# Kernel tuning notes

Hardware: AMD Instinct MI355X
Metric: run time of the kernel (lower is better)

## Reference

```python
import jax, jax.numpy as jnp
import numpy as np

H, C = 8, 8  # num_heads, c_hidden; c_m = H*C = 64
LN_EPS = 1e-5


def setup_inputs() -> dict:
    key = jax.random.key(0)
    ks = jax.random.split(key, 8)
    B, S, L, CM = 2, 512, 384, H * C
    m = jax.random.normal(ks[0], (B, S, L, CM), dtype=jnp.float32)
    msa_mask = jax.random.randint(ks[1], (B, S, L), 0, 2).astype(jnp.float32)
    sc = 1.0 / np.sqrt(CM)
    return {
        "m": m,
        "msa_mask": msa_mask,
        "ln_w": jnp.ones((CM,), jnp.float32),
        "ln_b": jnp.zeros((CM,), jnp.float32),
        "wq": jax.random.normal(ks[2], (CM, H * C), jnp.float32) * sc,
        "wk": jax.random.normal(ks[3], (CM, H * C), jnp.float32) * sc,
        "wv": jax.random.normal(ks[4], (CM, H * C), jnp.float32) * sc,
        "wg": jax.random.normal(ks[5], (CM, H * C), jnp.float32) * sc,
        "bg": jnp.ones((H * C,), jnp.float32),
        "wo": jax.random.normal(ks[6], (H * C, CM), jnp.float32) * sc,
        "bo": jnp.zeros((CM,), jnp.float32),
    }


def reference(m, msa_mask, ln_w, ln_b, wq, wk, wv, wg, bg, wo, bo):
    B, S, L, CM = m.shape
    # LayerNorm over c_m
    mu = jnp.mean(m, axis=-1, keepdims=True)
    var = jnp.mean(jnp.square(m - mu), axis=-1, keepdims=True)
    x = (m - mu) * jax.lax.rsqrt(var + LN_EPS) * ln_w + ln_b

    k = (x @ wk).reshape(B, S, L, H, C)
    v = (x @ wv).reshape(B, S, L, H, C)
    g = jax.nn.sigmoid(x @ wg + bg).reshape(B, S, L, H, C)

    # masked mean over the sequence axis S -> global query per residue
    denom = jnp.maximum(jnp.sum(msa_mask, axis=1), 1.0)  # [B, L]
    q_input = jnp.sum(x * msa_mask[..., None], axis=1) / denom[..., None]  # [B, L, CM]
    q = (q_input @ wq).reshape(B, L, H, C)

    logits = jnp.einsum("blhc,bslhc->blhs", q, k) / np.sqrt(C).astype(np.float32)
    mask_bls = jnp.transpose(msa_mask, (0, 2, 1))[:, :, None, :]  # [B, L, 1, S]
    logits = jnp.where(mask_bls == 0, -1e9, logits)
    attn = jax.nn.softmax(logits, axis=-1)  # [B, L, H, S]

    out_global = jnp.einsum("blhs,bslhc->blhc", attn, v)  # [B, L, H, C]
    out = g * out_global[:, None]  # broadcast over S -> [B, S, L, H, C]
    out = out.reshape(B, S, L, H * C) @ wo + bo
    out = out * msa_mask[..., None]
    return out
```

## Files before the change

### kernel.cpp

```cpp
#include <hip/hip_runtime.h>

#define NH 8
#define DCM 64
#define NB 2
#define NS 512
#define NL 384
#define LN_EPS 1e-5f
#define INV_SQRT_C 0.35355339059327379f

typedef __attribute__((ext_vector_type(8))) short short8v;
typedef __attribute__((ext_vector_type(4))) float f32x4;

__device__ __forceinline__ float4 ld4(const float* p) {
  return *reinterpret_cast<const float4*>(p);
}
__device__ __forceinline__ unsigned short f2bf(float f) {
  unsigned int b = __float_as_uint(f);
  b += 0x7FFFu + ((b >> 16) & 1u);
  return (unsigned short)(b >> 16);
}
__device__ __forceinline__ float bf2f(unsigned short u) {
  return __uint_as_float(((unsigned int)u) << 16);
}

__global__ void prep_weights(const float* __restrict__ wg,
                             const float* __restrict__ wo,
                             const float* __restrict__ wv,
                             unsigned short* __restrict__ wt) {
  int i = blockIdx.x * 256 + threadIdx.x;
  if (i < 4096) {
    int n = i >> 6, k = i & 63;
    wt[i]        = f2bf(wg[k * DCM + n]);
    wt[4096 + i] = f2bf(wo[k * DCM + n]);
    wt[8192 + i] = f2bf(wv[k * DCM + n]);
  }
}

__global__ __launch_bounds__(512, 2) void fused(
    const float* __restrict__ m, const float* __restrict__ msk,
    const float* __restrict__ lnw, const float* __restrict__ lnb,
    const float* __restrict__ wq, const float* __restrict__ wk,
    const unsigned short* __restrict__ wt,
    const float* __restrict__ bg, const float* __restrict__ bo,
    float* __restrict__ out)
{
  const int col = blockIdx.x;
  const int b = col / NL, l = col % NL;
  const int tid = threadIdx.x;
  const int wave = tid >> 6, lane = tid & 63;

  __shared__ __align__(16) unsigned short x_lds[NS * DCM];
  __shared__ __align__(16) unsigned short mask_s[NS];
  __shared__ __align__(16) unsigned char scratch[10752];
  __shared__ __align__(16) unsigned short qk_bf[16 * DCM];

  float* redf  = (float*)scratch;
  float* dredf = redf + 512;
  float* qinf  = redf + 528;
  float* qsf   = redf + 592;
  unsigned short* P_T = (unsigned short*)scratch;
  float* ogredf = (float*)(scratch + 8192);
  float* smredf = (float*)(scratch + 10240);
  float* ogsf   = (float*)(scratch + 10496);

  for (int i = tid; i < NS; i += 512)
    mask_s[i] = f2bf(msk[(b * NS + i) * NL + l]);

  const int c8 = lane & 7;
  const int r8 = lane >> 3;
  float lw8[8], lb8[8];
#pragma unroll
  for (int k = 0; k < 8; ++k) { lw8[k] = lnw[c8 * 8 + k]; lb8[k] = lnb[c8 * 8 + k]; }
  __syncthreads();

  float qacc[8] = {0.f,0.f,0.f,0.f,0.f,0.f,0.f,0.f};
  float dacc = 0.f;
  const int rowbase = wave * 64;
  {
    const size_t rstep = (size_t)8 * NL * DCM;
    const float* mb = m + ((size_t)b * NS * NL + l) * DCM + c8 * 8
                    + (size_t)(rowbase + r8) * NL * DCM;
    auto process = [&](const float4& A, const float4& Bv, int s) {
      float xv[8] = {A.x, A.y, A.z, A.w, Bv.x, Bv.y, Bv.z, Bv.w};
      float s1 = 0.f, s2 = 0.f;
#pragma unroll
      for (int k = 0; k < 8; ++k) { s1 += xv[k]; s2 += xv[k] * xv[k]; }
#pragma unroll
      for (int o = 1; o <= 4; o <<= 1) { s1 += __shfl_xor(s1, o); s2 += __shfl_xor(s2, o); }
      const float mu = s1 * 0.015625f;
      const float rs = rsqrtf(s2 * 0.015625f - mu * mu + LN_EPS);
      const float mk = bf2f(mask_s[s]);
      short8v xp;
#pragma unroll
      for (int k = 0; k < 8; ++k) {
        float xn = (xv[k] - mu) * rs * lw8[k] + lb8[k];
        xp[k] = (short)f2bf(xn);
        qacc[k] += xn * mk;
      }
      dacc += mk;
      *reinterpret_cast<short8v*>(&x_lds[s * DCM + ((c8 * 8) ^ ((s & 7) << 3))]) = xp;
    };
    float4 f0a = ld4(mb),             f0b = ld4(mb + 4);
    float4 f1a = ld4(mb + rstep),     f1b = ld4(mb + rstep + 4);
    float4 f2a = ld4(mb + 2 * rstep), f2b = ld4(mb + 2 * rstep + 4);
    float4 f3a = ld4(mb + 3 * rstep), f3b = ld4(mb + 3 * rstep + 4);
#pragma unroll
    for (int blk = 0; blk < 2; ++blk) {
      const int it0 = blk * 4;
      process(f0a, f0b, rowbase + (it0 + 0) * 8 + r8);
      if (blk < 1) { f0a = ld4(mb + (size_t)(it0 + 4) * rstep);
                     f0b = ld4(mb + (size_t)(it0 + 4) * rstep + 4); }
      process(f1a, f1b, rowbase + (it0 + 1) * 8 + r8);
      if (blk < 1) { f1a = ld4(mb + (size_t)(it0 + 5) * rstep);
                     f1b = ld4(mb + (size_t)(it0 + 5) * rstep + 4); }
      process(f2a, f2b, rowbase + (it0 + 2) * 8 + r8);
      if (blk < 1) { f2a = ld4(mb + (size_t)(it0 + 6) * rstep);
                     f2b = ld4(mb + (size_t)(it0 + 6) * rstep + 4); }
      process(f3a, f3b, rowbase + (it0 + 3) * 8 + r8);
      if (blk < 1) { f3a = ld4(mb + (size_t)(it0 + 7) * rstep);
                     f3b = ld4(mb + (size_t)(it0 + 7) * rstep + 4); }
    }
  }
#pragma unroll
  for (int o = 8; o <= 32; o <<= 1) {
#pragma unroll
    for (int k = 0; k < 8; ++k) qacc[k] += __shfl_xor(qacc[k], o);
    dacc += __shfl_xor(dacc, o);
  }
  if (lane < 8) {
    float4 t0; t0.x = qacc[0]; t0.y = qacc[1]; t0.z = qacc[2]; t0.w = qacc[3];
    float4 t1; t1.x = qacc[4]; t1.y = qacc[5]; t1.z = qacc[6]; t1.w = qacc[7];
    *reinterpret_cast<float4*>(&redf[wave * DCM + lane * 8])     = t0;
    *reinterpret_cast<float4*>(&redf[wave * DCM + lane * 8 + 4]) = t1;
  }
  if (lane == 0) dredf[wave] = dacc;
  __syncthreads();

  if (tid < DCM) {
    float dn = 0.f, a = 0.f;
#pragma unroll
    for (int w = 0; w < 8; ++w) { dn += dredf[w]; a += redf[w * DCM + tid]; }
    qinf[tid] = a / fmaxf(dn, 1.0f);
  }
  __syncthreads();
  if (tid < DCM) {
    float a = 0.f;
    for (int j = 0; j < DCM; ++j) a += qinf[j] * wq[j * DCM + tid];
    qsf[tid] = a;
  }
  __syncthreads();
  for (int idx = tid; idx < 16 * DCM; idx += 512) {
    int h = idx >> 6, cm = idx & 63;
    float a = 0.f;
    if (h < NH) {
#pragma unroll
      for (int c = 0; c < 8; ++c) a += qsf[h * 8 + c] * wk[cm * DCM + h * 8 + c];
      a *= INV_SQRT_C;
    }
    qk_bf[idx] = f2bf(a);
  }
  __syncthreads();

  const int bcol = lane & 15;
  const int kg = lane >> 4;
  short8v qkB0 = *reinterpret_cast<const short8v*>(&qk_bf[bcol * DCM + kg * 8]);
  short8v qkB1 = *reinterpret_cast<const short8v*>(&qk_bf[bcol * DCM + 32 + kg * 8]);
  short8v wvB[4][2];
#pragma unroll
  for (int nt = 0; nt < 4; ++nt)
#pragma unroll
    for (int kw = 0; kw < 2; ++kw)
      wvB[nt][kw] = *reinterpret_cast<const short8v*>(
          &wt[8192 + (nt * 16 + bcol) * DCM + kw * 32 + kg * 8]);
  float smacc = 0.f;
  float ogacc[4] = {0.f, 0.f, 0.f, 0.f};
  for (int t = 0; t < 4; ++t) {
    const int tilebase = rowbase + t * 16;
    const int arow = tilebase + bcol;
    const int swz = (arow & 7) << 3;
    short8v a0 = *reinterpret_cast<const short8v*>(&x_lds[arow * DCM + ((kg * 8) ^ swz)]);
    short8v a1 = *reinterpret_cast<const short8v*>(&x_lds[arow * DCM + ((32 + kg * 8) ^ swz)]);
    f32x4 L = (f32x4){0.f, 0.f, 0.f, 0.f};
    L = __builtin_amdgcn_mfma_f32_16x16x32_bf16(a0, qkB0, L, 0, 0, 0);
    L = __builtin_amdgcn_mfma_f32_16x16x32_bf16(a1, qkB1, L, 0, 0, 0);
    const int s0 = tilebase + kg * 4;
    short4 mk4 = *reinterpret_cast<const short4*>(&mask_s[s0]);
    float p0 = bf2f((unsigned short)mk4.x) * __expf(L[0]);
    float p1 = bf2f((unsigned short)mk4.y) * __expf(L[1]);
    float p2 = bf2f((unsigned short)mk4.z) * __expf(L[2]);
    float p3 = bf2f((unsigned short)mk4.w) * __expf(L[3]);
    smacc += (p0 + p1) + (p2 + p3);
    if (bcol < NH) {
      short4 pw;
      pw.x = (short)f2bf(p0); pw.y = (short)f2bf(p1);
      pw.z = (short)f2bf(p2); pw.w = (short)f2bf(p3);
      *reinterpret_cast<short4*>(&P_T[bcol * NS + (s0 ^ (bcol << 3))]) = pw;
    }
    f32x4 V[4];
#pragma unroll
    for (int nt = 0; nt < 4; ++nt) {
      V[nt] = (f32x4){0.f, 0.f, 0.f, 0.f};
      V[nt] = __builtin_amdgcn_mfma_f32_16x16x32_bf16(a0, wvB[nt][0], V[nt], 0, 0, 0);
      V[nt] = __builtin_amdgcn_mfma_f32_16x16x32_bf16(a1, wvB[nt][1], V[nt], 0, 0, 0);
    }
#pragma unroll
    for (int nt = 0; nt < 4; ++nt) {
      const int h2 = 2 * nt + (bcol >> 3);
      short4 p4 = *reinterpret_cast<const short4*>(&P_T[h2 * NS + (s0 ^ (h2 << 3))]);
      ogacc[nt] += bf2f((unsigned short)p4.x) * V[nt][0]
                 + bf2f((unsigned short)p4.y) * V[nt][1]
                 + bf2f((unsigned short)p4.z) * V[nt][2]
                 + bf2f((unsigned short)p4.w) * V[nt][3];
    }
  }
  smacc += __shfl_xor(smacc, 16); smacc += __shfl_xor(smacc, 32);
  if (lane < NH) smredf[wave * NH + lane] = smacc;
#pragma unroll
  for (int nt = 0; nt < 4; ++nt) {
    ogacc[nt] += __shfl_xor(ogacc[nt], 16);
    ogacc[nt] += __shfl_xor(ogacc[nt], 32);
  }
  if (lane < 16) {
#pragma unroll
    for (int nt = 0; nt < 4; ++nt) ogredf[wave * DCM + nt * 16 + lane] = ogacc[nt];
  }
  __syncthreads();
  if (tid < DCM) {
    float smT = 0.f, a = 0.f;
#pragma unroll
    for (int w = 0; w < 8; ++w) {
      smT += smredf[w * NH + (tid >> 3)];
      a += ogredf[w * DCM + tid];
    }
    ogsf[tid] = a / fmaxf(smT, 1e-30f);
  }
  __syncthreads();

  short8v wgB[4][2], woB[4][2];
  float bgv[4], bov[4], ogv[4];
#pragma unroll
  for (int nt = 0; nt < 4; ++nt) {
    const int ncol = nt * 16 + bcol;
#pragma unroll
    for (int kw = 0; kw < 2; ++kw) {
      wgB[nt][kw] = *reinterpret_cast<const short8v*>(&wt[ncol * DCM + kw * 32 + kg * 8]);
      woB[nt][kw] = *reinterpret_cast<const short8v*>(&wt[4096 + ncol * DCM + kw * 32 + kg * 8]);
    }
    bgv[nt] = bg[ncol]; bov[nt] = bo[ncol]; ogv[nt] = ogsf[ncol];
  }
  const size_t outbase = ((size_t)b * NS * NL + l) * DCM;

  for (int t = 0; t < 4; ++t) {
    const int tilebase = rowbase + t * 16;
    const int arow = tilebase + bcol;
    const int swz = (arow & 7) << 3;
    short8v a0 = *reinterpret_cast<const short8v*>(&x_lds[arow * DCM + ((kg * 8) ^ swz)]);
    short8v a1 = *reinterpret_cast<const short8v*>(&x_lds[arow * DCM + ((32 + kg * 8) ^ swz)]);
    f32x4 accG[4];
#pragma unroll
    for (int nt = 0; nt < 4; ++nt) {
      accG[nt] = (f32x4){0.f, 0.f, 0.f, 0.f};
      accG[nt] = __builtin_amdgcn_mfma_f32_16x16x32_bf16(a0, wgB[nt][0], accG[nt], 0, 0, 0);
      accG[nt] = __builtin_amdgcn_mfma_f32_16x16x32_bf16(a1, wgB[nt][1], accG[nt], 0, 0, 0);
    }
#pragma unroll
    for (int nt = 0; nt < 4; ++nt) {
      const int cc = nt * 16 + bcol;
#pragma unroll
      for (int r = 0; r < 4; ++r) {
        const int r2 = kg * 4 + r;
        float gx = accG[nt][r] + bgv[nt];
        float g = 1.0f / (1.0f + __expf(-gx));
        x_lds[(tilebase + r2) * DCM + (cc ^ ((r2 & 7) << 3))] = f2bf(g * ogv[nt]);
      }
    }
    short8v b0 = *reinterpret_cast<const short8v*>(
        &x_lds[(tilebase + bcol) * DCM + ((kg * 8) ^ ((bcol & 7) << 3))]);
    short8v b1 = *reinterpret_cast<const short8v*>(
        &x_lds[(tilebase + bcol) * DCM + ((32 + kg * 8) ^ ((bcol & 7) << 3))]);
    f32x4 accO[4];
#pragma unroll
    for (int nt = 0; nt < 4; ++nt) {
      accO[nt] = (f32x4){0.f, 0.f, 0.f, 0.f};
      accO[nt] = __builtin_amdgcn_mfma_f32_16x16x32_bf16(b0, woB[nt][0], accO[nt], 0, 0, 0);
      accO[nt] = __builtin_amdgcn_mfma_f32_16x16x32_bf16(b1, woB[nt][1], accO[nt], 0, 0, 0);
    }
#pragma unroll
    for (int nt = 0; nt < 4; ++nt) {
#pragma unroll
      for (int r = 0; r < 4; ++r) {
        const int orow = tilebase + kg * 4 + r;
        const float mk = bf2f(mask_s[orow]);
        out[outbase + (size_t)orow * NL * DCM + nt * 16 + bcol] = (accO[nt][r] + bov[nt]) * mk;
      }
    }
  }
}

extern "C" void kernel_launch(void* const* d_in, const int* in_sizes, int n_in,
                              void* d_out, int out_size, void* d_ws, size_t ws_size,
                              hipStream_t stream) {
  (void)in_sizes; (void)n_in; (void)out_size; (void)ws_size;
  const float* m   = (const float*)d_in[0];
  const float* msk = (const float*)d_in[1];
  const float* lnw = (const float*)d_in[2];
  const float* lnb = (const float*)d_in[3];
  const float* wq  = (const float*)d_in[4];
  const float* wk  = (const float*)d_in[5];
  const float* wv  = (const float*)d_in[6];
  const float* wg  = (const float*)d_in[7];
  const float* bg  = (const float*)d_in[8];
  const float* wo  = (const float*)d_in[9];
  const float* bo  = (const float*)d_in[10];
  unsigned short* wt = (unsigned short*)d_ws;
  float* out = (float*)d_out;

  prep_weights<<<dim3(16), dim3(256), 0, stream>>>(wg, wo, wv, wt);
  fused<<<dim3(NB * NL), dim3(512), 0, stream>>>(
      m, msk, lnw, lnb, wq, wk, wt, bg, bo, out);
}
```

Baseline: 79.77 us.

## Precompute fused Wq·Wk product, row-per-thread LayerNorm, halve block size

Precomputes the combined query-key projection matrix (wq times per-head wk, scaled) in the prep kernel, so the fused kernel turns the masked-mean input into qk logit weights with one 64x512 matvec and no serial wq/wk passes. LayerNorm is rewritten so each thread owns one full row (16 float4 loads) with no shuffle reductions. The masked query sum is recomputed from the bf16 x_lds. Blocks shrink from 512 to 256 threads with each wave covering 128 rows. This trades per-row shuffle work and extra syncs for more register pressure and lower bf16 precision in q_input.

```diff
diff --git a/kernel.cpp b/kernel.cpp
--- a/kernel.cpp
+++ b/kernel.cpp
@@ -23,10 +23,10 @@
   return __uint_as_float(((unsigned int)u) << 16);
 }
 
-__global__ void prep_weights(const float* __restrict__ wg,
-                             const float* __restrict__ wo,
-                             const float* __restrict__ wv,
-                             unsigned short* __restrict__ wt) {
+__global__ void prep(const float* __restrict__ wg, const float* __restrict__ wo,
+                     const float* __restrict__ wv, const float* __restrict__ wq,
+                     const float* __restrict__ wk,
+                     unsigned short* __restrict__ wt, float* __restrict__ Mg) {
   int i = blockIdx.x * 256 + threadIdx.x;
   if (i < 4096) {
     int n = i >> 6, k = i & 63;
@@ -34,13 +34,19 @@
     wt[4096 + i] = f2bf(wo[k * DCM + n]);
     wt[8192 + i] = f2bf(wv[k * DCM + n]);
   }
-}
-
-__global__ __launch_bounds__(512, 2) void fused(
+  if (i < 32768) {
+    int j = i >> 9, idx = i & 511, h = idx >> 6, cm = idx & 63;
+    float a = 0.f;
+#pragma unroll
+    for (int c = 0; c < 8; ++c) a += wq[j * DCM + h * 8 + c] * wk[cm * DCM + h * 8 + c];
+    Mg[i] = a * INV_SQRT_C;
+  }
+}
+
+__global__ __launch_bounds__(256, 4) void fused(
     const float* __restrict__ m, const float* __restrict__ msk,
     const float* __restrict__ lnw, const float* __restrict__ lnb,
-    const float* __restrict__ wq, const float* __restrict__ wk,
-    const unsigned short* __restrict__ wt,
+    const unsigned short* __restrict__ wt, const float* __restrict__ Mg,
     const float* __restrict__ bg, const float* __restrict__ bo,
     float* __restrict__ out)
 {
@@ -51,118 +57,94 @@
 
   __shared__ __align__(16) unsigned short x_lds[NS * DCM];
   __shared__ __align__(16) unsigned short mask_s[NS];
-  __shared__ __align__(16) unsigned char scratch[10752];
+  __shared__ __align__(16) unsigned char scratch[9728];
   __shared__ __align__(16) unsigned short qk_bf[16 * DCM];
 
   float* redf  = (float*)scratch;
-  float* dredf = redf + 512;
-  float* qinf  = redf + 528;
-  float* qsf   = redf + 592;
+  float* dredf = (float*)(scratch + 1024);
   unsigned short* P_T = (unsigned short*)scratch;
   float* ogredf = (float*)(scratch + 8192);
-  float* smredf = (float*)(scratch + 10240);
-  float* ogsf   = (float*)(scratch + 10496);
-
-  for (int i = tid; i < NS; i += 512)
+  float* smredf = (float*)(scratch + 9216);
+  float* ogsf   = (float*)(scratch + 9344);
+
+  for (int i = tid; i < NS; i += 256)
     mask_s[i] = f2bf(msk[(b * NS + i) * NL + l]);
 
-  const int c8 = lane & 7;
-  const int r8 = lane >> 3;
-  float lw8[8], lb8[8];
-#pragma unroll
-  for (int k = 0; k < 8; ++k) { lw8[k] = lnw[c8 * 8 + k]; lb8[k] = lnb[c8 * 8 + k]; }
-  __syncthreads();
-
-  float qacc[8] = {0.f,0.f,0.f,0.f,0.f,0.f,0.f,0.f};
-  float dacc = 0.f;
-  const int rowbase = wave * 64;
+#pragma unroll 1
+  for (int rr = 0; rr < 2; ++rr) {
+    const int r = tid + rr * 256;
+    const float* rp = m + ((size_t)(b * NS + r) * NL + l) * DCM;
+    float4 f[16];
+#pragma unroll
+    for (int j = 0; j < 16; ++j) f[j] = ld4(rp + j * 4);
+    float s1 = 0.f, s2 = 0.f;
+#pragma unroll
+    for (int j = 0; j < 16; ++j) {
+      s1 += (f[j].x + f[j].y) + (f[j].z + f[j].w);
+      s2 = fmaf(f[j].x, f[j].x, s2); s2 = fmaf(f[j].y, f[j].y, s2);
+      s2 = fmaf(f[j].z, f[j].z, s2); s2 = fmaf(f[j].w, f[j].w, s2);
+    }
+    const float mu = s1 * 0.015625f;
+    const float rs = rsqrtf(s2 * 0.015625f - mu * mu + LN_EPS);
+    const int swz = (r & 7) << 3;
+#pragma unroll
+    for (int j = 0; j < 8; ++j) {
+      const float v[8] = {f[2*j].x, f[2*j].y, f[2*j].z, f[2*j].w,
+                          f[2*j+1].x, f[2*j+1].y, f[2*j+1].z, f[2*j+1].w};
+      short8v xp;
+#pragma unroll
+      for (int k = 0; k < 8; ++k)
+        xp[k] = (short)f2bf((v[k] - mu) * rs * lnw[8*j+k] + lnb[8*j+k]);
+      *reinterpret_cast<short8v*>(&x_lds[r * DCM + ((j * 8) ^ swz)]) = xp;
+    }
+  }
+  __syncthreads();
+
+  const int qd = lane & 15, rsub = lane >> 4;
   {
-    const size_t rstep = (size_t)8 * NL * DCM;
-    const float* mb = m + ((size_t)b * NS * NL + l) * DCM + c8 * 8
-                    + (size_t)(rowbase + r8) * NL * DCM;
-    auto process = [&](const float4& A, const float4& Bv, int s) {
-      float xv[8] = {A.x, A.y, A.z, A.w, Bv.x, Bv.y, Bv.z, Bv.w};
-      float s1 = 0.f, s2 = 0.f;
-#pragma unroll
-      for (int k = 0; k < 8; ++k) { s1 += xv[k]; s2 += xv[k] * xv[k]; }
-#pragma unroll
-      for (int o = 1; o <= 4; o <<= 1) { s1 += __shfl_xor(s1, o); s2 += __shfl_xor(s2, o); }
-      const float mu = s1 * 0.015625f;
-      const float rs = rsqrtf(s2 * 0.015625f - mu * mu + LN_EPS);
+    float q0 = 0.f, q1 = 0.f, q2 = 0.f, q3 = 0.f, da = 0.f;
+    for (int it = 0; it < 32; ++it) {
+      const int s = wave * 4 + rsub + it * 16;
+      short4 xv4 = *reinterpret_cast<const short4*>(
+          &x_lds[s * DCM + ((qd * 4) ^ ((s & 7) << 3))]);
       const float mk = bf2f(mask_s[s]);
-      short8v xp;
-#pragma unroll
-      for (int k = 0; k < 8; ++k) {
-        float xn = (xv[k] - mu) * rs * lw8[k] + lb8[k];
-        xp[k] = (short)f2bf(xn);
-        qacc[k] += xn * mk;
-      }
-      dacc += mk;
-      *reinterpret_cast<short8v*>(&x_lds[s * DCM + ((c8 * 8) ^ ((s & 7) << 3))]) = xp;
-    };
-    float4 f0a = ld4(mb),             f0b = ld4(mb + 4);
-    float4 f1a = ld4(mb + rstep),     f1b = ld4(mb + rstep + 4);
-    float4 f2a = ld4(mb + 2 * rstep), f2b = ld4(mb + 2 * rstep + 4);
-    float4 f3a = ld4(mb + 3 * rstep), f3b = ld4(mb + 3 * rstep + 4);
-#pragma unroll
-    for (int blk = 0; blk < 2; ++blk) {
-      const int it0 = blk * 4;
-      process(f0a, f0b, rowbase + (it0 + 0) * 8 + r8);
-      if (blk < 1) { f0a = ld4(mb + (size_t)(it0 + 4) * rstep);
-                     f0b = ld4(mb + (size_t)(it0 + 4) * rstep + 4); }
-      process(f1a, f1b, rowbase + (it0 + 1) * 8 + r8);
-      if (blk < 1) { f1a = ld4(mb + (size_t)(it0 + 5) * rstep);
-                     f1b = ld4(mb + (size_t)(it0 + 5) * rstep + 4); }
-      process(f2a, f2b, rowbase + (it0 + 2) * 8 + r8);
-      if (blk < 1) { f2a = ld4(mb + (size_t)(it0 + 6) * rstep);
-                     f2b = ld4(mb + (size_t)(it0 + 6) * rstep + 4); }
-      process(f3a, f3b, rowbase + (it0 + 3) * 8 + r8);
-      if (blk < 1) { f3a = ld4(mb + (size_t)(it0 + 7) * rstep);
-                     f3b = ld4(mb + (size_t)(it0 + 7) * rstep + 4); }
-    }
-  }
-#pragma unroll
-  for (int o = 8; o <= 32; o <<= 1) {
-#pragma unroll
-    for (int k = 0; k < 8; ++k) qacc[k] += __shfl_xor(qacc[k], o);
-    dacc += __shfl_xor(dacc, o);
-  }
-  if (lane < 8) {
-    float4 t0; t0.x = qacc[0]; t0.y = qacc[1]; t0.z = qacc[2]; t0.w = qacc[3];
-    float4 t1; t1.x = qacc[4]; t1.y = qacc[5]; t1.z = qacc[6]; t1.w = qacc[7];
-    *reinterpret_cast<float4*>(&redf[wave * DCM + lane * 8])     = t0;
-    *reinterpret_cast<float4*>(&redf[wave * DCM + lane * 8 + 4]) = t1;
-  }
-  if (lane == 0) dredf[wave] = dacc;
-  __syncthreads();
-
-  if (tid < DCM) {
-    float dn = 0.f, a = 0.f;
-#pragma unroll
-    for (int w = 0; w < 8; ++w) { dn += dredf[w]; a += redf[w * DCM + tid]; }
-    qinf[tid] = a / fmaxf(dn, 1.0f);
-  }
-  __syncthreads();
-  if (tid < DCM) {
-    float a = 0.f;
-    for (int j = 0; j < DCM; ++j) a += qinf[j] * wq[j * DCM + tid];
-    qsf[tid] = a;
-  }
-  __syncthreads();
-  for (int idx = tid; idx < 16 * DCM; idx += 512) {
-    int h = idx >> 6, cm = idx & 63;
-    float a = 0.f;
-    if (h < NH) {
-#pragma unroll
-      for (int c = 0; c < 8; ++c) a += qsf[h * 8 + c] * wk[cm * DCM + h * 8 + c];
-      a *= INV_SQRT_C;
-    }
-    qk_bf[idx] = f2bf(a);
+      q0 = fmaf(mk, bf2f((unsigned short)xv4.x), q0);
+      q1 = fmaf(mk, bf2f((unsigned short)xv4.y), q1);
+      q2 = fmaf(mk, bf2f((unsigned short)xv4.z), q2);
+      q3 = fmaf(mk, bf2f((unsigned short)xv4.w), q3);
+      da += mk;
+    }
+    q0 += __shfl_xor(q0, 16); q0 += __shfl_xor(q0, 32);
+    q1 += __shfl_xor(q1, 16); q1 += __shfl_xor(q1, 32);
+    q2 += __shfl_xor(q2, 16); q2 += __shfl_xor(q2, 32);
+    q3 += __shfl_xor(q3, 16); q3 += __shfl_xor(q3, 32);
+    da += __shfl_xor(da, 16); da += __shfl_xor(da, 32);
+    if (lane < 16) {
+      float4 t; t.x = q0; t.y = q1; t.z = q2; t.w = q3;
+      *reinterpret_cast<float4*>(&redf[wave * DCM + qd * 4]) = t;
+    }
+    if (lane == 0) dredf[wave] = da;
+    qk_bf[512 + tid] = 0;
+    qk_bf[768 + tid] = 0;
+  }
+  __syncthreads();
+
+  {
+    const float inv_dn = 1.0f / fmaxf((dredf[0] + dredf[1]) + (dredf[2] + dredf[3]), 1.0f);
+    float a0 = 0.f, a1 = 0.f;
+    for (int j = 0; j < 64; ++j) {
+      const float qs = (redf[j] + redf[64 + j]) + (redf[128 + j] + redf[192 + j]);
+      a0 = fmaf(qs, Mg[j * 512 + tid], a0);
+      a1 = fmaf(qs, Mg[j * 512 + tid + 256], a1);
+    }
+    qk_bf[tid]       = f2bf(a0 * inv_dn);
+    qk_bf[tid + 256] = f2bf(a1 * inv_dn);
   }
   __syncthreads();
 
   const int bcol = lane & 15;
   const int kg = lane >> 4;
+  const int rowbase = wave * 128;
   short8v qkB0 = *reinterpret_cast<const short8v*>(&qk_bf[bcol * DCM + kg * 8]);
   short8v qkB1 = *reinterpret_cast<const short8v*>(&qk_bf[bcol * DCM + 32 + kg * 8]);
   short8v wvB[4][2];
@@ -174,7 +156,7 @@
           &wt[8192 + (nt * 16 + bcol) * DCM + kw * 32 + kg * 8]);
   float smacc = 0.f;
   float ogacc[4] = {0.f, 0.f, 0.f, 0.f};
-  for (int t = 0; t < 4; ++t) {
+  for (int t = 0; t < 8; ++t) {
     const int tilebase = rowbase + t * 16;
     const int arow = tilebase + bcol;
     const int swz = (arow & 7) << 3;
@@ -228,7 +210,7 @@
   if (tid < DCM) {
     float smT = 0.f, a = 0.f;
 #pragma unroll
-    for (int w = 0; w < 8; ++w) {
+    for (int w = 0; w < 4; ++w) {
       smT += smredf[w * NH + (tid >> 3)];
       a += ogredf[w * DCM + tid];
     }
@@ -250,7 +232,7 @@
   }
   const size_t outbase = ((size_t)b * NS * NL + l) * DCM;
 
-  for (int t = 0; t < 4; ++t) {
+  for (int t = 0; t < 8; ++t) {
     const int tilebase = rowbase + t * 16;
     const int arow = tilebase + bcol;
     const int swz = (arow & 7) << 3;
@@ -313,9 +295,10 @@
   const float* wo  = (const float*)d_in[9];
   const float* bo  = (const float*)d_in[10];
   unsigned short* wt = (unsigned short*)d_ws;
+  float* Mg = (float*)((char*)d_ws + 24576);
   float* out = (float*)d_out;
 
-  prep_weights<<<dim3(16), dim3(256), 0, stream>>>(wg, wo, wv, wt);
-  fused<<<dim3(NB * NL), dim3(512), 0, stream>>>(
-      m, msk, lnw, lnb, wq, wk, wt, bg, bo, out);
-}
+  prep<<<dim3(128), dim3(256), 0, stream>>>(wg, wo, wv, wq, wk, wt, Mg);
+  fused<<<dim3(NB * NL), dim3(256), 0, stream>>>(
+      m, msk, lnw, lnb, wt, Mg, bg, bo, out);
+}
```

After: 93.07 us. 16.7% more time.

## Precompute fused Wq·Wk matrix and halve block size to 256 threads

Applied to the files above, without the earlier changes.

Folds the Wq and Wk projections into one precomputed 64x512 matrix in the prep kernel, so each block does a single GEMV from the pooled query input instead of two serial reductions with extra barriers. The fused kernel now runs with 4 waves of 256 threads, each handling 128 rows, and the gated activations go to a per-wave scratch tile instead of being written back into x_lds. Fewer threads per block means less parallelism per column but lighter barriers, and LDS use may allow more blocks per CU. It also switches the bf16 conversion to the library intrinsic and uses explicit fma.

```diff
diff --git a/kernel.cpp b/kernel.cpp
--- a/kernel.cpp
+++ b/kernel.cpp
@@ -1,4 +1,5 @@
 #include <hip/hip_runtime.h>
+#include <hip/hip_bf16.h>
 
 #define NH 8
 #define DCM 64
@@ -15,18 +16,17 @@
   return *reinterpret_cast<const float4*>(p);
 }
 __device__ __forceinline__ unsigned short f2bf(float f) {
-  unsigned int b = __float_as_uint(f);
-  b += 0x7FFFu + ((b >> 16) & 1u);
-  return (unsigned short)(b >> 16);
+  __hip_bfloat16 h = __float2bfloat16(f);
+  return __builtin_bit_cast(unsigned short, h);
 }
 __device__ __forceinline__ float bf2f(unsigned short u) {
   return __uint_as_float(((unsigned int)u) << 16);
 }
 
-__global__ void prep_weights(const float* __restrict__ wg,
-                             const float* __restrict__ wo,
-                             const float* __restrict__ wv,
-                             unsigned short* __restrict__ wt) {
+__global__ void prep(const float* __restrict__ wg, const float* __restrict__ wo,
+                     const float* __restrict__ wv, const float* __restrict__ wq,
+                     const float* __restrict__ wk,
+                     unsigned short* __restrict__ wt, float* __restrict__ Mg) {
   int i = blockIdx.x * 256 + threadIdx.x;
   if (i < 4096) {
     int n = i >> 6, k = i & 63;
@@ -34,13 +34,19 @@
     wt[4096 + i] = f2bf(wo[k * DCM + n]);
     wt[8192 + i] = f2bf(wv[k * DCM + n]);
   }
-}
-
-__global__ __launch_bounds__(512, 2) void fused(
+  if (i < 32768) {
+    int j = i >> 9, idx = i & 511, h = idx >> 6, cm = idx & 63;
+    float a = 0.f;
+#pragma unroll
+    for (int c = 0; c < 8; ++c) a += wq[j * DCM + h * 8 + c] * wk[cm * DCM + h * 8 + c];
+    Mg[i] = a * INV_SQRT_C;
+  }
+}
+
+__global__ __launch_bounds__(256) void fused(
     const float* __restrict__ m, const float* __restrict__ msk,
     const float* __restrict__ lnw, const float* __restrict__ lnb,
-    const float* __restrict__ wq, const float* __restrict__ wk,
-    const unsigned short* __restrict__ wt,
+    const unsigned short* __restrict__ wt, const float* __restrict__ Mg,
     const float* __restrict__ bg, const float* __restrict__ bo,
     float* __restrict__ out)
 {
@@ -51,23 +57,23 @@
 
   __shared__ __align__(16) unsigned short x_lds[NS * DCM];
   __shared__ __align__(16) unsigned short mask_s[NS];
-  __shared__ __align__(16) unsigned char scratch[10752];
+  __shared__ __align__(16) unsigned char scratch[8192];
   __shared__ __align__(16) unsigned short qk_bf[16 * DCM];
-
-  float* redf  = (float*)scratch;
-  float* dredf = redf + 512;
-  float* qinf  = redf + 528;
-  float* qsf   = redf + 592;
+  __shared__ __align__(16) float ogredf[4 * DCM];
+  __shared__ float smredf[4 * NH];
+  __shared__ float ogsf[DCM];
+  __shared__ float dredf[4];
+
+  float* redf = (float*)scratch;
   unsigned short* P_T = (unsigned short*)scratch;
-  float* ogredf = (float*)(scratch + 8192);
-  float* smredf = (float*)(scratch + 10240);
-  float* ogsf   = (float*)(scratch + 10496);
-
-  for (int i = tid; i < NS; i += 512)
+  unsigned short* a2t = (unsigned short*)scratch;
+
+  for (int i = tid; i < NS; i += 256)
     mask_s[i] = f2bf(msk[(b * NS + i) * NL + l]);
 
   const int c8 = lane & 7;
   const int r8 = lane >> 3;
+  const float* mbase = m + ((size_t)b * NS * NL + l) * DCM + c8 * 8;
   float lw8[8], lb8[8];
 #pragma unroll
   for (int k = 0; k < 8; ++k) { lw8[k] = lnw[c8 * 8 + k]; lb8[k] = lnb[c8 * 8 + k]; }
@@ -75,16 +81,15 @@
 
   float qacc[8] = {0.f,0.f,0.f,0.f,0.f,0.f,0.f,0.f};
   float dacc = 0.f;
-  const int rowbase = wave * 64;
+  const int rowbase = wave * 128;
   {
     const size_t rstep = (size_t)8 * NL * DCM;
-    const float* mb = m + ((size_t)b * NS * NL + l) * DCM + c8 * 8
-                    + (size_t)(rowbase + r8) * NL * DCM;
+    const float* mb = mbase + (size_t)(rowbase + r8) * NL * DCM;
     auto process = [&](const float4& A, const float4& Bv, int s) {
       float xv[8] = {A.x, A.y, A.z, A.w, Bv.x, Bv.y, Bv.z, Bv.w};
       float s1 = 0.f, s2 = 0.f;
 #pragma unroll
-      for (int k = 0; k < 8; ++k) { s1 += xv[k]; s2 += xv[k] * xv[k]; }
+      for (int k = 0; k < 8; ++k) { s1 += xv[k]; s2 = fmaf(xv[k], xv[k], s2); }
 #pragma unroll
       for (int o = 1; o <= 4; o <<= 1) { s1 += __shfl_xor(s1, o); s2 += __shfl_xor(s2, o); }
       const float mu = s1 * 0.015625f;
@@ -95,7 +100,7 @@
       for (int k = 0; k < 8; ++k) {
         float xn = (xv[k] - mu) * rs * lw8[k] + lb8[k];
         xp[k] = (short)f2bf(xn);
-        qacc[k] += xn * mk;
+        qacc[k] = fmaf(xn, mk, qacc[k]);
       }
       dacc += mk;
       *reinterpret_cast<short8v*>(&x_lds[s * DCM + ((c8 * 8) ^ ((s & 7) << 3))]) = xp;
@@ -105,19 +110,19 @@
     float4 f2a = ld4(mb + 2 * rstep), f2b = ld4(mb + 2 * rstep + 4);
     float4 f3a = ld4(mb + 3 * rstep), f3b = ld4(mb + 3 * rstep + 4);
 #pragma unroll
-    for (int blk = 0; blk < 2; ++blk) {
+    for (int blk = 0; blk < 4; ++blk) {
       const int it0 = blk * 4;
       process(f0a, f0b, rowbase + (it0 + 0) * 8 + r8);
-      if (blk < 1) { f0a = ld4(mb + (size_t)(it0 + 4) * rstep);
+      if (blk < 3) { f0a = ld4(mb + (size_t)(it0 + 4) * rstep);
                      f0b = ld4(mb + (size_t)(it0 + 4) * rstep + 4); }
       process(f1a, f1b, rowbase + (it0 + 1) * 8 + r8);
-      if (blk < 1) { f1a = ld4(mb + (size_t)(it0 + 5) * rstep);
+      if (blk < 3) { f1a = ld4(mb + (size_t)(it0 + 5) * rstep);
                      f1b = ld4(mb + (size_t)(it0 + 5) * rstep + 4); }
       process(f2a, f2b, rowbase + (it0 + 2) * 8 + r8);
-      if (blk < 1) { f2a = ld4(mb + (size_t)(it0 + 6) * rstep);
+      if (blk < 3) { f2a = ld4(mb + (size_t)(it0 + 6) * rstep);
                      f2b = ld4(mb + (size_t)(it0 + 6) * rstep + 4); }
       process(f3a, f3b, rowbase + (it0 + 3) * 8 + r8);
-      if (blk < 1) { f3a = ld4(mb + (size_t)(it0 + 7) * rstep);
+      if (blk < 3) { f3a = ld4(mb + (size_t)(it0 + 7) * rstep);
                      f3b = ld4(mb + (size_t)(it0 + 7) * rstep + 4); }
     }
   }
@@ -136,28 +141,18 @@
   if (lane == 0) dredf[wave] = dacc;
   __syncthreads();
 
-  if (tid < DCM) {
-    float dn = 0.f, a = 0.f;
-#pragma unroll
-    for (int w = 0; w < 8; ++w) { dn += dredf[w]; a += redf[w * DCM + tid]; }
-    qinf[tid] = a / fmaxf(dn, 1.0f);
-  }
-  __syncthreads();
-  if (tid < DCM) {
-    float a = 0.f;
-    for (int j = 0; j < DCM; ++j) a += qinf[j] * wq[j * DCM + tid];
-    qsf[tid] = a;
-  }
-  __syncthreads();
-  for (int idx = tid; idx < 16 * DCM; idx += 512) {
-    int h = idx >> 6, cm = idx & 63;
-    float a = 0.f;
-    if (h < NH) {
-#pragma unroll
-      for (int c = 0; c < 8; ++c) a += qsf[h * 8 + c] * wk[cm * DCM + h * 8 + c];
-      a *= INV_SQRT_C;
-    }
-    qk_bf[idx] = f2bf(a);
+  {
+    const float inv_dn = 1.0f / fmaxf((dredf[0] + dredf[1]) + (dredf[2] + dredf[3]), 1.0f);
+    float a0 = 0.f, a1 = 0.f;
+    for (int j = 0; j < 64; ++j) {
+      const float qs = (redf[j] + redf[64 + j]) + (redf[128 + j] + redf[192 + j]);
+      a0 = fmaf(qs, Mg[j * 512 + tid], a0);
+      a1 = fmaf(qs, Mg[j * 512 + tid + 256], a1);
+    }
+    qk_bf[tid]       = f2bf(a0 * inv_dn);
+    qk_bf[tid + 256] = f2bf(a1 * inv_dn);
+    qk_bf[tid + 512] = 0;
+    qk_bf[tid + 768] = 0;
   }
   __syncthreads();
 
@@ -174,7 +169,7 @@
           &wt[8192 + (nt * 16 + bcol) * DCM + kw * 32 + kg * 8]);
   float smacc = 0.f;
   float ogacc[4] = {0.f, 0.f, 0.f, 0.f};
-  for (int t = 0; t < 4; ++t) {
+  for (int t = 0; t < 8; ++t) {
     const int tilebase = rowbase + t * 16;
     const int arow = tilebase + bcol;
     const int swz = (arow & 7) << 3;
@@ -228,7 +223,7 @@
   if (tid < DCM) {
     float smT = 0.f, a = 0.f;
 #pragma unroll
-    for (int w = 0; w < 8; ++w) {
+    for (int w = 0; w < 4; ++w) {
       smT += smredf[w * NH + (tid >> 3)];
       a += ogredf[w * DCM + tid];
     }
@@ -249,8 +244,9 @@
     bgv[nt] = bg[ncol]; bov[nt] = bo[ncol]; ogv[nt] = ogsf[ncol];
   }
   const size_t outbase = ((size_t)b * NS * NL + l) * DCM;
-
-  for (int t = 0; t < 4; ++t) {
+  unsigned short* a2w = &a2t[wave * 16 * DCM];
+
+  for (int t = 0; t < 8; ++t) {
     const int tilebase = rowbase + t * 16;
     const int arow = tilebase + bcol;
     const int swz = (arow & 7) << 3;
@@ -271,13 +267,13 @@
         const int r2 = kg * 4 + r;
         float gx = accG[nt][r] + bgv[nt];
         float g = 1.0f / (1.0f + __expf(-gx));
-        x_lds[(tilebase + r2) * DCM + (cc ^ ((r2 & 7) << 3))] = f2bf(g * ogv[nt]);
+        a2w[r2 * DCM + (cc ^ ((r2 & 7) << 3))] = f2bf(g * ogv[nt]);
       }
     }
     short8v b0 = *reinterpret_cast<const short8v*>(
-        &x_lds[(tilebase + bcol) * DCM + ((kg * 8) ^ ((bcol & 7) << 3))]);
+        &a2w[bcol * DCM + ((kg * 8) ^ ((bcol & 7) << 3))]);
     short8v b1 = *reinterpret_cast<const short8v*>(
-        &x_lds[(tilebase + bcol) * DCM + ((32 + kg * 8) ^ ((bcol & 7) << 3))]);
+        &a2w[bcol * DCM + ((32 + kg * 8) ^ ((bcol & 7) << 3))]);
     f32x4 accO[4];
 #pragma unroll
     for (int nt = 0; nt < 4; ++nt) {
@@ -313,9 +309,10 @@
   const float* wo  = (const float*)d_in[9];
   const float* bo  = (const float*)d_in[10];
   unsigned short* wt = (unsigned short*)d_ws;
+  float* Mg = (float*)((char*)d_ws + 24576);
   float* out = (float*)d_out;
 
-  prep_weights<<<dim3(16), dim3(256), 0, stream>>>(wg, wo, wv, wt);
-  fused<<<dim3(NB * NL), dim3(512), 0, stream>>>(
-      m, msk, lnw, lnb, wq, wk, wt, bg, bo, out);
-}
+  prep<<<dim3(128), dim3(256), 0, stream>>>(wg, wo, wv, wq, wk, wt, Mg);
+  fused<<<dim3(NB * NL), dim3(256), 0, stream>>>(
+      m, msk, lnw, lnb, wt, Mg, bg, bo, out);
+}
```

Result: slower. 86.28 us (+8.2%).
